# Kernel tuning notes

Hardware: AMD Instinct MI355X
Metric: run time of the kernel (lower is better)

Reference implementation:

```python
import jax, jax.numpy as jnp
import numpy as np

WS = 12      # window_size
OV = 6       # overlap
STEP = WS - OV
EPS = 1e-5   # LayerNorm eps (torch default)


def setup_inputs() -> dict:
    key = jax.random.key(0)
    ks = jax.random.split(key, 6)
    B, L, H, Dh = 4, 4092, 8, 64
    d_model = H * Dh
    sc = 1.0 / np.sqrt(Dh)
    return {
        "queries": jax.random.normal(ks[0], (B, L, H, Dh), dtype=jnp.float32),
        "keys": jax.random.normal(ks[1], (B, L, H, Dh), dtype=jnp.float32),
        "values": jax.random.normal(ks[2], (B, L, H, Dh), dtype=jnp.float32),
        "Wq": jax.random.normal(ks[3], (Dh, Dh), dtype=jnp.float32) * sc,
        "Wk": jax.random.normal(ks[4], (Dh, Dh), dtype=jnp.float32) * sc,
        "Wv": jax.random.normal(ks[5], (Dh, Dh), dtype=jnp.float32) * sc,
        "gamma": jnp.ones((d_model,), dtype=jnp.float32),
        "beta": jnp.zeros((d_model,), dtype=jnp.float32),
    }


def reference(queries, keys, values, Wq, Wk, Wv, gamma, beta):
    # input layout: [B, L, H, Dh]
    B, L, H, Dh = queries.shape
    nw = (L - OV) // STEP                       # number of windows
    Lc = WS + STEP * (nw - 1)                   # reconstructed length (== L)
    idx = jnp.arange(nw)[:, None] * STEP + jnp.arange(WS)[None, :]  # [nw, WS]

    def windows(x):
        # [B,L,H,Dh] -> [B,H,nw,WS,Dh]
        return jnp.transpose(x, (0, 2, 1, 3))[:, :, idx, :]

    qw, kw, vw = windows(queries), windows(keys), windows(values)
    # per-head-dim linear projections (nn.Linear: x @ W.T)
    Q = jnp.einsum('bhnwd,ed->bhnwe', qw, Wq)
    K = jnp.einsum('bhnwd,ed->bhnwe', kw, Wk)
    V = jnp.einsum('bhnwd,ed->bhnwe', vw, Wv)

    scores = jnp.einsum('bhnqd,bhnkd->bhnqk', Q, K) / jnp.sqrt(jnp.asarray(Dh, Q.dtype))
    attn = jax.nn.softmax(scores, axis=-1)      # [B,H,nw,WS,WS]
    ow = jnp.einsum('bhnqk,bhnkd->bhnqd', attn, V)

    # [B,H,nw,WS,Dh] -> [B,nw,WS,H*Dh]
    attn_out = jnp.transpose(ow, (0, 2, 3, 1, 4)).reshape(B, nw, WS, H * Dh)

    # overlap-add + averaging
    flat_idx = idx.reshape(-1)                  # [nw*WS]
    acc = jnp.zeros((B, Lc, H * Dh), dtype=attn_out.dtype)
    acc = acc.at[:, flat_idx, :].add(attn_out.reshape(B, nw * WS, H * Dh))
    cnt = jnp.zeros((Lc,), dtype=attn_out.dtype).at[flat_idx].add(1.0)
    out = acc / cnt[None, :, None]

    # residual + LayerNorm
    resid = queries.reshape(B, L, H * Dh)
    x = out + resid
    mu = jnp.mean(x, axis=-1, keepdims=True)
    var = jnp.mean((x - mu) ** 2, axis=-1, keepdims=True)
    z = (x - mu) / jnp.sqrt(var + EPS) * gamma + beta
    return z, attn
```

## Files before the change

### kernel.cpp

```cpp
#include <hip/hip_runtime.h>
#include <math.h>

#define B_    4
#define L_    4092
#define H_    8
#define DM    512
#define WS_   12
#define NW    681
#define NC    682
#define NC2   341
#define EPS_  1e-5f
#define Z_ELEMS (B_*L_*DM)

typedef unsigned short u16;
typedef __attribute__((ext_vector_type(8))) short short8;
typedef __attribute__((ext_vector_type(4))) float floatx4;

__device__ __forceinline__ u16 f2bf(float f) {
    union { float f; unsigned u; } x; x.f = f;
    unsigned u = x.u;
    return (u16)((u + 0x7FFFu + ((u >> 16) & 1u)) >> 16);
}
__device__ __forceinline__ float bf2f(u16 h) {
    union { unsigned u; float f; } x; x.u = ((unsigned)h) << 16; return x.f;
}
__device__ __forceinline__ void pack8_hl(float4 a, float4 b, short8& hi, short8& lo) {
    float v[8] = {a.x, a.y, a.z, a.w, b.x, b.y, b.z, b.w};
    #pragma unroll
    for (int i = 0; i < 8; ++i) {
        u16 h = f2bf(v[i]);
        hi[i] = (short)h;
        lo[i] = (short)f2bf(v[i] - bf2f(h));
    }
}

__global__ __launch_bounds__(256) void proj_kernel(
    const float* __restrict__ q, const float* __restrict__ k, const float* __restrict__ v,
    const float* __restrict__ Wq, const float* __restrict__ Wk, const float* __restrict__ Wv,
    float* __restrict__ Qf, float* __restrict__ Kf, u16* __restrict__ Vh)
{
    const int tensor = blockIdx.y;
    const float* __restrict__ X = (tensor == 0) ? q  : (tensor == 1) ? k  : v;
    const float* __restrict__ W = (tensor == 0) ? Wq : (tensor == 1) ? Wk : Wv;
    float* __restrict__ Yf      = (tensor == 0) ? Qf : Kf;
    const bool isV = (tensor == 2);

    const int t = threadIdx.x, lane = t & 63, wv = t >> 6;
    const int m = lane & 15, q3 = lane >> 4;

    short8 wfh[4][2], wfl[4][2];
    #pragma unroll
    for (int nt = 0; nt < 4; ++nt)
        #pragma unroll
        for (int kc = 0; kc < 2; ++kc) {
            const float* wp = W + (4 * m + nt) * 64 + kc * 32 + q3 * 8;
            pack8_hl(*(const float4*)wp, *(const float4*)(wp + 4), wfh[nt][kc], wfl[nt][kc]);
        }

    const int waveId = blockIdx.x * 4 + wv;
    for (int tile = waveId; tile < 8184; tile += 2048) {
        const int rbase = tile * 16;
        const int r = rbase + m;
        const int bh = r / L_;
        const int l = r - bh * L_;
        const int b = bh >> 3, h = bh & 7;
        const float* xp = X + (((size_t)b * L_ + l) * H_ + h) * 64;
        short8 a0h, a0l, a1h, a1l;
        pack8_hl(*(const float4*)(xp + q3 * 8),      *(const float4*)(xp + q3 * 8 + 4),      a0h, a0l);
        pack8_hl(*(const float4*)(xp + 32 + q3 * 8), *(const float4*)(xp + 32 + q3 * 8 + 4), a1h, a1l);

        floatx4 acc[4];
        #pragma unroll
        for (int nt = 0; nt < 4; ++nt) {
            floatx4 c = {0.f, 0.f, 0.f, 0.f};
            c = __builtin_amdgcn_mfma_f32_16x16x32_bf16(a0h, wfh[nt][0], c, 0, 0, 0);
            c = __builtin_amdgcn_mfma_f32_16x16x32_bf16(a1h, wfh[nt][1], c, 0, 0, 0);
            c = __builtin_amdgcn_mfma_f32_16x16x32_bf16(a0h, wfl[nt][0], c, 0, 0, 0);
            c = __builtin_amdgcn_mfma_f32_16x16x32_bf16(a0l, wfh[nt][0], c, 0, 0, 0);
            c = __builtin_amdgcn_mfma_f32_16x16x32_bf16(a1h, wfl[nt][1], c, 0, 0, 0);
            c = __builtin_amdgcn_mfma_f32_16x16x32_bf16(a1l, wfh[nt][1], c, 0, 0, 0);
            acc[nt] = c;
        }
        #pragma unroll
        for (int reg = 0; reg < 4; ++reg) {
            const int row = rbase + q3 * 4 + reg;
            if (!isV) {
                float4 o4;
                o4.x = acc[0][reg]; o4.y = acc[1][reg];
                o4.z = acc[2][reg]; o4.w = acc[3][reg];
                *(float4*)(Yf + (size_t)row * 64 + 4 * m) = o4;
            } else {
                ushort4 o4;
                o4.x = f2bf(acc[0][reg]); o4.y = f2bf(acc[1][reg]);
                o4.z = f2bf(acc[2][reg]); o4.w = f2bf(acc[3][reg]);
                *(ushort4*)(Vh + (size_t)row * 64 + 4 * m) = o4;
            }
        }
    }
}

__global__ __launch_bounds__(256, 3) void attn_kernel(
    const float* __restrict__ Qf, const float* __restrict__ Kf, const u16* __restrict__ Vh,
    float* __restrict__ attn, float* __restrict__ xout)
{
    __shared__ alignas(16) float Ks[4][24][64];
    __shared__ alignas(16) float Vs[4][24][64];

    const int c2 = blockIdx.x, b = blockIdx.y, hg = blockIdx.z;
    const int t = threadIdx.x, lane = t & 63, w = t >> 6;
    const int h = hg * 4 + w;
    const int qq = lane >> 2, ks = lane & 3;
    const int bh = b * 8 + h;
    const int lbase = c2 * 12 - 6;

    for (int i = t; i < 1536; i += 256) {
        const int hh  = i / 384;
        const int rem = i - hh * 384;
        const int rr  = rem >> 4;
        const int cc  = (rem & 15) * 4;
        const int l = lbase + rr;
        float4 kf4 = make_float4(0.f, 0.f, 0.f, 0.f);
        float4 vf4 = make_float4(0.f, 0.f, 0.f, 0.f);
        if (l >= 0 && l < L_) {
            const size_t base = ((size_t)(b * 8 + hg * 4 + hh) * L_ + l) * 64 + cc;
            kf4 = *(const float4*)(Kf + base);
            const ushort4 u4 = *(const ushort4*)(Vh + base);
            vf4.x = bf2f(u4.x); vf4.y = bf2f(u4.y); vf4.z = bf2f(u4.z); vf4.w = bf2f(u4.w);
        }
        *(float4*)&Ks[hh][rr][cc] = kf4;
        *(float4*)&Vs[hh][rr][cc] = vf4;
    }
    __syncthreads();

    #pragma unroll
    for (int j = 0; j < 2; ++j) {
        const int c = c2 * 2 + j;
        const bool hasA = (c < NW), hasB = (c > 0);
        const float scale = (hasA && hasB) ? 0.5f : 1.0f;
        const int koff = 6 * j;

        float4 qs0, qs1, qs2, qs3;
        const int qmax = hasA ? 12 : 6;
        if (qq < qmax) {
            const float* qp = Qf + ((size_t)bh * L_ + (c * 6 + qq)) * 64 + ks * 16;
            qs0 = *(const float4*)(qp);     qs1 = *(const float4*)(qp + 4);
            qs2 = *(const float4*)(qp + 8); qs3 = *(const float4*)(qp + 12);
        } else {
            qs0 = qs1 = qs2 = qs3 = make_float4(0.f, 0.f, 0.f, 0.f);
        }

        float s[18];
        #pragma unroll
        for (int kt = 0; kt < 18; ++kt) {
            const float* kp = &Ks[w][koff + kt][ks * 16];
            const float4 k0 = *(const float4*)(kp);
            const float4 k1 = *(const float4*)(kp + 4);
            const float4 k2 = *(const float4*)(kp + 8);
            const float4 k3 = *(const float4*)(kp + 12);
            s[kt] = qs0.x*k0.x + qs0.y*k0.y + qs0.z*k0.z + qs0.w*k0.w
                  + qs1.x*k1.x + qs1.y*k1.y + qs1.z*k1.z + qs1.w*k1.w
                  + qs2.x*k2.x + qs2.y*k2.y + qs2.z*k2.z + qs2.w*k2.w
                  + qs3.x*k3.x + qs3.y*k3.y + qs3.z*k3.z + qs3.w*k3.w;
        }
        #pragma unroll
        for (int kt = 0; kt < 18; ++kt) {
            s[kt] += __shfl_xor(s[kt], 1);
            s[kt] += __shfl_xor(s[kt], 2);
        }

        float eA[12], invA = 0.f;
        if (hasA) {
            float mxA = s[6];
            #pragma unroll
            for (int jj = 1; jj < 12; ++jj) mxA = fmaxf(mxA, s[6 + jj]);
            float sumA = 0.f;
            #pragma unroll
            for (int jj = 0; jj < 12; ++jj) { eA[jj] = __expf((s[6 + jj] - mxA) * 0.125f); sumA += eA[jj]; }
            invA = 1.0f / sumA;
            if (ks == 0 && qq < 12) {
                float* ao = attn + ((size_t)bh * NW + c) * 144 + qq * 12;
                float4 a0, a1, a2;
                a0.x = eA[0]*invA; a0.y = eA[1]*invA;  a0.z = eA[2]*invA;  a0.w = eA[3]*invA;
                a1.x = eA[4]*invA; a1.y = eA[5]*invA;  a1.z = eA[6]*invA;  a1.w = eA[7]*invA;
                a2.x = eA[8]*invA; a2.y = eA[9]*invA;  a2.z = eA[10]*invA; a2.w = eA[11]*invA;
                *(float4*)(ao)     = a0;
                *(float4*)(ao + 4) = a1;
                *(float4*)(ao + 8) = a2;
            }
        } else {
            #pragma unroll
            for (int jj = 0; jj < 12; ++jj) eA[jj] = 0.f;
        }

        float eB[12], invB = 0.f;
        if (hasB) {
            float mxB = s[0];
            #pragma unroll
            for (int jj = 1; jj < 12; ++jj) mxB = fmaxf(mxB, s[jj]);
            float sumB = 0.f;
            #pragma unroll
            for (int jj = 0; jj < 12; ++jj) { eB[jj] = __expf((s[jj] - mxB) * 0.125f); sumB += eB[jj]; }
            invB = 1.0f / sumB;
        } else {
            #pragma unroll
            for (int jj = 0; jj < 12; ++jj) eB[jj] = 0.f;
        }

        if (qq < 6) {
            float4 xo0 = make_float4(0.f,0.f,0.f,0.f), xo1 = xo0, xo2 = xo0, xo3 = xo0;
            #pragma unroll
            for (int kt = 0; kt < 18; ++kt) {
                const float wa = (kt >= 6) ? eA[kt - 6] * invA : 0.f;
                const float wb = (kt < 12) ? eB[kt] * invB : 0.f;
                const float wk = scale * (wa + wb);
                const float* vp = &Vs[w][koff + kt][ks * 16];
                const float4 v0 = *(const float4*)(vp);
                const float4 v1 = *(const float4*)(vp + 4);
                const float4 v2 = *(const float4*)(vp + 8);
                const float4 v3 = *(const float4*)(vp + 12);
                xo0.x += wk*v0.x; xo0.y += wk*v0.y; xo0.z += wk*v0.z; xo0.w += wk*v0.w;
                xo1.x += wk*v1.x; xo1.y += wk*v1.y; xo1.z += wk*v1.z; xo1.w += wk*v1.w;
                xo2.x += wk*v2.x; xo2.y += wk*v2.y; xo2.z += wk*v2.z; xo2.w += wk*v2.w;
                xo3.x += wk*v3.x; xo3.y += wk*v3.y; xo3.z += wk*v3.z; xo3.w += wk*v3.w;
            }
            float* xp = xout + ((size_t)b * L_ + (c * 6 + qq)) * DM + h * 64 + ks * 16;
            *(float4*)(xp)      = xo0;
            *(float4*)(xp + 4)  = xo1;
            *(float4*)(xp + 8)  = xo2;
            *(float4*)(xp + 12) = xo3;
        }
    }
}

__global__ __launch_bounds__(512) void ln_kernel(
    const float* __restrict__ qres, const float* __restrict__ gamma,
    const float* __restrict__ beta, float* __restrict__ z)
{
    const int row = blockIdx.x * 8 + (threadIdx.x >> 6);
    const int lane = threadIdx.x & 63;
    const int cc = lane * 8;

    float* xp = z + (size_t)row * DM + cc;
    float4 xa = *(const float4*)(xp);
    float4 xb = *(const float4*)(xp + 4);
    const float* qr = qres + (size_t)row * DM + cc;
    const float4 ra  = *(const float4*)qr;
    const float4 rb2 = *(const float4*)(qr + 4);
    xa.x += ra.x;  xa.y += ra.y;  xa.z += ra.z;  xa.w += ra.w;
    xb.x += rb2.x; xb.y += rb2.y; xb.z += rb2.z; xb.w += rb2.w;

    float s1 = xa.x + xa.y + xa.z + xa.w + xb.x + xb.y + xb.z + xb.w;
    float s2 = xa.x*xa.x + xa.y*xa.y + xa.z*xa.z + xa.w*xa.w
             + xb.x*xb.x + xb.y*xb.y + xb.z*xb.z + xb.w*xb.w;
    #pragma unroll
    for (int off = 1; off < 64; off <<= 1) {
        s1 += __shfl_xor(s1, off, 64);
        s2 += __shfl_xor(s2, off, 64);
    }
    const float mu  = s1 * (1.0f / 512.0f);
    const float var = s2 * (1.0f / 512.0f) - mu * mu;
    const float inv = 1.0f / sqrtf(var + EPS_);

    const float4 ga = *(const float4*)(gamma + cc);
    const float4 gb = *(const float4*)(gamma + cc + 4);
    const float4 ba = *(const float4*)(beta + cc);
    const float4 bb = *(const float4*)(beta + cc + 4);
    float4 oa, ob;
    oa.x = (xa.x - mu) * inv * ga.x + ba.x;
    oa.y = (xa.y - mu) * inv * ga.y + ba.y;
    oa.z = (xa.z - mu) * inv * ga.z + ba.z;
    oa.w = (xa.w - mu) * inv * ga.w + ba.w;
    ob.x = (xb.x - mu) * inv * gb.x + bb.x;
    ob.y = (xb.y - mu) * inv * gb.y + bb.y;
    ob.z = (xb.z - mu) * inv * gb.z + bb.z;
    ob.w = (xb.w - mu) * inv * gb.w + bb.w;
    *(float4*)(xp)     = oa;
    *(float4*)(xp + 4) = ob;
}

extern "C" void kernel_launch(void* const* d_in, const int* in_sizes, int n_in,
                              void* d_out, int out_size, void* d_ws, size_t ws_size,
                              hipStream_t stream) {
    const float* q     = (const float*)d_in[0];
    const float* k     = (const float*)d_in[1];
    const float* v     = (const float*)d_in[2];
    const float* Wq    = (const float*)d_in[3];
    const float* Wk    = (const float*)d_in[4];
    const float* Wv    = (const float*)d_in[5];
    const float* gamma = (const float*)d_in[6];
    const float* beta  = (const float*)d_in[7];

    float* z    = (float*)d_out;
    float* attn = (float*)d_out + Z_ELEMS;

    const size_t plane = (size_t)B_ * H_ * L_ * 64;
    float* Qf = (float*)d_ws;
    float* Kf = Qf + plane;
    u16*  Vh  = (u16*)(Kf + plane);

    proj_kernel<<<dim3(512, 3, 1), 256, 0, stream>>>(q, k, v, Wq, Wk, Wv, Qf, Kf, Vh);
    attn_kernel<<<dim3(NC2, B_, 2), 256, 0, stream>>>(Qf, Kf, Vh, attn, z);
    ln_kernel<<<dim3(2046, 1, 1), 512, 0, stream>>>(q, gamma, beta, z);
}
```

Baseline: 227.1 us.

## Store V as bf16 in LDS, split PV across lanes, batch LN rows, widen proj grid

The attention kernel now keeps V as bf16 in shared memory, which halves LDS use and allows a higher occupancy hint. The 18-row PV accumulation is split between two lane groups, with weights exchanged and partial sums combined through shuffles, so that otherwise idle lanes (qq>=6) do work. The LayerNorm kernel processes two rows per wave to add memory-level parallelism, and the projection grid is doubled so each wave handles fewer tiles. The cost is extra shuffles and index logic, plus the risk of register pressure under the tighter launch bound.

```diff
diff --git a/kernel.cpp b/kernel.cpp
--- a/kernel.cpp
+++ b/kernel.cpp
@@ -24,6 +24,12 @@
 __device__ __forceinline__ float bf2f(u16 h) {
     union { unsigned u; float f; } x; x.u = ((unsigned)h) << 16; return x.f;
 }
+__device__ __forceinline__ float lo16f(unsigned u) {
+    union { unsigned x; float f; } a; a.x = u << 16; return a.f;
+}
+__device__ __forceinline__ float hi16f(unsigned u) {
+    union { unsigned x; float f; } a; a.x = u & 0xffff0000u; return a.f;
+}
 __device__ __forceinline__ void pack8_hl(float4 a, float4 b, short8& hi, short8& lo) {
     float v[8] = {a.x, a.y, a.z, a.w, b.x, b.y, b.z, b.w};
     #pragma unroll
@@ -58,7 +64,7 @@
         }
 
     const int waveId = blockIdx.x * 4 + wv;
-    for (int tile = waveId; tile < 8184; tile += 2048) {
+    for (int tile = waveId; tile < 8184; tile += 4096) {
         const int rbase = tile * 16;
         const int r = rbase + m;
         const int bh = r / L_;
@@ -99,12 +105,12 @@
     }
 }
 
-__global__ __launch_bounds__(256, 3) void attn_kernel(
+__global__ __launch_bounds__(256, 4) void attn_kernel(
     const float* __restrict__ Qf, const float* __restrict__ Kf, const u16* __restrict__ Vh,
     float* __restrict__ attn, float* __restrict__ xout)
 {
     __shared__ alignas(16) float Ks[4][24][64];
-    __shared__ alignas(16) float Vs[4][24][64];
+    __shared__ alignas(16) u16  Vs16[4][24][64];
 
     const int c2 = blockIdx.x, b = blockIdx.y, hg = blockIdx.z;
     const int t = threadIdx.x, lane = t & 63, w = t >> 6;
@@ -120,15 +126,14 @@
         const int cc  = (rem & 15) * 4;
         const int l = lbase + rr;
         float4 kf4 = make_float4(0.f, 0.f, 0.f, 0.f);
-        float4 vf4 = make_float4(0.f, 0.f, 0.f, 0.f);
+        ushort4 v4 = {0, 0, 0, 0};
         if (l >= 0 && l < L_) {
             const size_t base = ((size_t)(b * 8 + hg * 4 + hh) * L_ + l) * 64 + cc;
             kf4 = *(const float4*)(Kf + base);
-            const ushort4 u4 = *(const ushort4*)(Vh + base);
-            vf4.x = bf2f(u4.x); vf4.y = bf2f(u4.y); vf4.z = bf2f(u4.z); vf4.w = bf2f(u4.w);
-        }
-        *(float4*)&Ks[hh][rr][cc] = kf4;
-        *(float4*)&Vs[hh][rr][cc] = vf4;
+            v4  = *(const ushort4*)(Vh + base);
+        }
+        *(float4*)&Ks[hh][rr][cc]   = kf4;
+        *(ushort4*)&Vs16[hh][rr][cc] = v4;
     }
     __syncthreads();
 
@@ -206,23 +211,47 @@
             for (int jj = 0; jj < 12; ++jj) eB[jj] = 0.f;
         }
 
+        float wk[18];
+        #pragma unroll
+        for (int kt = 0; kt < 18; ++kt) {
+            const float wa = (kt >= 6) ? eA[kt - 6] * invA : 0.f;
+            const float wb = (kt < 12) ? eB[kt] * invB : 0.f;
+            wk[kt] = scale * (wa + wb);
+        }
+        const int srcW = (lane >= 24 && lane < 48) ? lane - 24 : lane;
+        #pragma unroll
+        for (int kk = 0; kk < 9; ++kk)
+            wk[9 + kk] = __shfl(wk[9 + kk], srcW);
+
+        const int grp = (lane < 24) ? 0 : 1;
+        const u16* vrow = &Vs16[w][koff][0] + (grp ? 9 * 64 : 0) + ks * 16;
+        float4 xo0 = make_float4(0.f,0.f,0.f,0.f), xo1 = xo0, xo2 = xo0, xo3 = xo0;
+        #pragma unroll
+        for (int kk = 0; kk < 9; ++kk) {
+            const float wkv = grp ? wk[9 + kk] : wk[kk];
+            const u16* vp = vrow + kk * 64;
+            const uint4 ua = *(const uint4*)(vp);
+            const uint4 ub = *(const uint4*)(vp + 8);
+            xo0.x += wkv * lo16f(ua.x); xo0.y += wkv * hi16f(ua.x);
+            xo0.z += wkv * lo16f(ua.y); xo0.w += wkv * hi16f(ua.y);
+            xo1.x += wkv * lo16f(ua.z); xo1.y += wkv * hi16f(ua.z);
+            xo1.z += wkv * lo16f(ua.w); xo1.w += wkv * hi16f(ua.w);
+            xo2.x += wkv * lo16f(ub.x); xo2.y += wkv * hi16f(ub.x);
+            xo2.z += wkv * lo16f(ub.y); xo2.w += wkv * hi16f(ub.y);
+            xo3.x += wkv * lo16f(ub.z); xo3.y += wkv * hi16f(ub.z);
+            xo3.z += wkv * lo16f(ub.w); xo3.w += wkv * hi16f(ub.w);
+        }
+        const int srcC = (lane < 24) ? lane + 24 : lane;
+        xo0.x += __shfl(xo0.x, srcC); xo0.y += __shfl(xo0.y, srcC);
+        xo0.z += __shfl(xo0.z, srcC); xo0.w += __shfl(xo0.w, srcC);
+        xo1.x += __shfl(xo1.x, srcC); xo1.y += __shfl(xo1.y, srcC);
+        xo1.z += __shfl(xo1.z, srcC); xo1.w += __shfl(xo1.w, srcC);
+        xo2.x += __shfl(xo2.x, srcC); xo2.y += __shfl(xo2.y, srcC);
+        xo2.z += __shfl(xo2.z, srcC); xo2.w += __shfl(xo2.w, srcC);
+        xo3.x += __shfl(xo3.x, srcC); xo3.y += __shfl(xo3.y, srcC);
+        xo3.z += __shfl(xo3.z, srcC); xo3.w += __shfl(xo3.w, srcC);
+
         if (qq < 6) {
-            float4 xo0 = make_float4(0.f,0.f,0.f,0.f), xo1 = xo0, xo2 = xo0, xo3 = xo0;
-            #pragma unroll
-            for (int kt = 0; kt < 18; ++kt) {
-                const float wa = (kt >= 6) ? eA[kt - 6] * invA : 0.f;
-                const float wb = (kt < 12) ? eB[kt] * invB : 0.f;
-                const float wk = scale * (wa + wb);
-                const float* vp = &Vs[w][koff + kt][ks * 16];
-                const float4 v0 = *(const float4*)(vp);
-                const float4 v1 = *(const float4*)(vp + 4);
-                const float4 v2 = *(const float4*)(vp + 8);
-                const float4 v3 = *(const float4*)(vp + 12);
-                xo0.x += wk*v0.x; xo0.y += wk*v0.y; xo0.z += wk*v0.z; xo0.w += wk*v0.w;
-                xo1.x += wk*v1.x; xo1.y += wk*v1.y; xo1.z += wk*v1.z; xo1.w += wk*v1.w;
-                xo2.x += wk*v2.x; xo2.y += wk*v2.y; xo2.z += wk*v2.z; xo2.w += wk*v2.w;
-                xo3.x += wk*v3.x; xo3.y += wk*v3.y; xo3.z += wk*v3.z; xo3.w += wk*v3.w;
-            }
             float* xp = xout + ((size_t)b * L_ + (c * 6 + qq)) * DM + h * 64 + ks * 16;
             *(float4*)(xp)      = xo0;
             *(float4*)(xp + 4)  = xo1;
@@ -236,46 +265,75 @@
     const float* __restrict__ qres, const float* __restrict__ gamma,
     const float* __restrict__ beta, float* __restrict__ z)
 {
-    const int row = blockIdx.x * 8 + (threadIdx.x >> 6);
-    const int lane = threadIdx.x & 63;
+    const int wv = threadIdx.x >> 6, lane = threadIdx.x & 63;
+    const int row0 = (blockIdx.x * 8 + wv) * 2;
     const int cc = lane * 8;
 
-    float* xp = z + (size_t)row * DM + cc;
-    float4 xa = *(const float4*)(xp);
-    float4 xb = *(const float4*)(xp + 4);
-    const float* qr = qres + (size_t)row * DM + cc;
-    const float4 ra  = *(const float4*)qr;
-    const float4 rb2 = *(const float4*)(qr + 4);
-    xa.x += ra.x;  xa.y += ra.y;  xa.z += ra.z;  xa.w += ra.w;
-    xb.x += rb2.x; xb.y += rb2.y; xb.z += rb2.z; xb.w += rb2.w;
-
-    float s1 = xa.x + xa.y + xa.z + xa.w + xb.x + xb.y + xb.z + xb.w;
-    float s2 = xa.x*xa.x + xa.y*xa.y + xa.z*xa.z + xa.w*xa.w
-             + xb.x*xb.x + xb.y*xb.y + xb.z*xb.z + xb.w*xb.w;
-    #pragma unroll
-    for (int off = 1; off < 64; off <<= 1) {
-        s1 += __shfl_xor(s1, off, 64);
-        s2 += __shfl_xor(s2, off, 64);
-    }
-    const float mu  = s1 * (1.0f / 512.0f);
-    const float var = s2 * (1.0f / 512.0f) - mu * mu;
-    const float inv = 1.0f / sqrtf(var + EPS_);
-
+    float* xp0 = z + (size_t)row0 * DM + cc;
+    float* xp1 = z + (size_t)(row0 + 1) * DM + cc;
+    const float* qr0 = qres + (size_t)row0 * DM + cc;
+    const float* qr1 = qres + (size_t)(row0 + 1) * DM + cc;
+
+    float4 xa0 = *(const float4*)(xp0);
+    float4 xb0 = *(const float4*)(xp0 + 4);
+    float4 xa1 = *(const float4*)(xp1);
+    float4 xb1 = *(const float4*)(xp1 + 4);
+    const float4 ra0  = *(const float4*)qr0;
+    const float4 rb0  = *(const float4*)(qr0 + 4);
+    const float4 ra1  = *(const float4*)qr1;
+    const float4 rb1  = *(const float4*)(qr1 + 4);
     const float4 ga = *(const float4*)(gamma + cc);
     const float4 gb = *(const float4*)(gamma + cc + 4);
     const float4 ba = *(const float4*)(beta + cc);
     const float4 bb = *(const float4*)(beta + cc + 4);
+
+    xa0.x += ra0.x; xa0.y += ra0.y; xa0.z += ra0.z; xa0.w += ra0.w;
+    xb0.x += rb0.x; xb0.y += rb0.y; xb0.z += rb0.z; xb0.w += rb0.w;
+    xa1.x += ra1.x; xa1.y += ra1.y; xa1.z += ra1.z; xa1.w += ra1.w;
+    xb1.x += rb1.x; xb1.y += rb1.y; xb1.z += rb1.z; xb1.w += rb1.w;
+
+    float s10 = xa0.x + xa0.y + xa0.z + xa0.w + xb0.x + xb0.y + xb0.z + xb0.w;
+    float s20 = xa0.x*xa0.x + xa0.y*xa0.y + xa0.z*xa0.z + xa0.w*xa0.w
+              + xb0.x*xb0.x + xb0.y*xb0.y + xb0.z*xb0.z + xb0.w*xb0.w;
+    float s11 = xa1.x + xa1.y + xa1.z + xa1.w + xb1.x + xb1.y + xb1.z + xb1.w;
+    float s21 = xa1.x*xa1.x + xa1.y*xa1.y + xa1.z*xa1.z + xa1.w*xa1.w
+              + xb1.x*xb1.x + xb1.y*xb1.y + xb1.z*xb1.z + xb1.w*xb1.w;
+    #pragma unroll
+    for (int off = 1; off < 64; off <<= 1) {
+        s10 += __shfl_xor(s10, off, 64);
+        s20 += __shfl_xor(s20, off, 64);
+        s11 += __shfl_xor(s11, off, 64);
+        s21 += __shfl_xor(s21, off, 64);
+    }
+    const float mu0  = s10 * (1.0f / 512.0f);
+    const float var0 = s20 * (1.0f / 512.0f) - mu0 * mu0;
+    const float inv0 = 1.0f / sqrtf(var0 + EPS_);
+    const float mu1  = s11 * (1.0f / 512.0f);
+    const float var1 = s21 * (1.0f / 512.0f) - mu1 * mu1;
+    const float inv1 = 1.0f / sqrtf(var1 + EPS_);
+
     float4 oa, ob;
-    oa.x = (xa.x - mu) * inv * ga.x + ba.x;
-    oa.y = (xa.y - mu) * inv * ga.y + ba.y;
-    oa.z = (xa.z - mu) * inv * ga.z + ba.z;
-    oa.w = (xa.w - mu) * inv * ga.w + ba.w;
-    ob.x = (xb.x - mu) * inv * gb.x + bb.x;
-    ob.y = (xb.y - mu) * inv * gb.y + bb.y;
-    ob.z = (xb.z - mu) * inv * gb.z + bb.z;
-    ob.w = (xb.w - mu) * inv * gb.w + bb.w;
-    *(float4*)(xp)     = oa;
-    *(float4*)(xp + 4) = ob;
+    oa.x = (xa0.x - mu0) * inv0 * ga.x + ba.x;
+    oa.y = (xa0.y - mu0) * inv0 * ga.y + ba.y;
+    oa.z = (xa0.z - mu0) * inv0 * ga.z + ba.z;
+    oa.w = (xa0.w - mu0) * inv0 * ga.w + ba.w;
+    ob.x = (xb0.x - mu0) * inv0 * gb.x + bb.x;
+    ob.y = (xb0.y - mu0) * inv0 * gb.y + bb.y;
+    ob.z = (xb0.z - mu0) * inv0 * gb.z + bb.z;
+    ob.w = (xb0.w - mu0) * inv0 * gb.w + bb.w;
+    *(float4*)(xp0)     = oa;
+    *(float4*)(xp0 + 4) = ob;
+
+    oa.x = (xa1.x - mu1) * inv1 * ga.x + ba.x;
+    oa.y = (xa1.y - mu1) * inv1 * ga.y + ba.y;
+    oa.z = (xa1.z - mu1) * inv1 * ga.z + ba.z;
+    oa.w = (xa1.w - mu1) * inv1 * ga.w + ba.w;
+    ob.x = (xb1.x - mu1) * inv1 * gb.x + bb.x;
+    ob.y = (xb1.y - mu1) * inv1 * gb.y + bb.y;
+    ob.z = (xb1.z - mu1) * inv1 * gb.z + bb.z;
+    ob.w = (xb1.w - mu1) * inv1 * gb.w + bb.w;
+    *(float4*)(xp1)     = oa;
+    *(float4*)(xp1 + 4) = ob;
 }
 
 extern "C" void kernel_launch(void* const* d_in, const int* in_sizes, int n_in,
@@ -298,7 +356,7 @@
     float* Kf = Qf + plane;
     u16*  Vh  = (u16*)(Kf + plane);
 
-    proj_kernel<<<dim3(512, 3, 1), 256, 0, stream>>>(q, k, v, Wq, Wk, Wv, Qf, Kf, Vh);
+    proj_kernel<<<dim3(1024, 3, 1), 256, 0, stream>>>(q, k, v, Wq, Wk, Wv, Qf, Kf, Vh);
     attn_kernel<<<dim3(NC2, B_, 2), 256, 0, stream>>>(Qf, Kf, Vh, attn, z);
-    ln_kernel<<<dim3(2046, 1, 1), 512, 0, stream>>>(q, gamma, beta, z);
-}
+    ln_kernel<<<dim3(1023, 1, 1), 512, 0, stream>>>(q, gamma, beta, z);
+}
```

After: 284.7 us. 25.4% more time.
